# Performance work log

Measured on AMD Instinct MI355X. Metric: run time of the kernel, lower is better.

Reference implementation:

```python
import jax, jax.numpy as jnp
import numpy as np

B, T, D, K = 4, 4096, 384, 64

def setup_inputs() -> dict:
    key = jax.random.key(0)
    k1, k2, k3, k4 = jax.random.split(key, 4)
    x = jax.random.normal(k1, (B, T, D), dtype=jnp.float32)
    # nn.Linear weights stored as (out_features, in_features); y = x @ W.T
    Wk = jax.random.normal(k2, (K, D), dtype=jnp.float32) * (1.0 / np.sqrt(D))
    Wq = jax.random.normal(k3, (K, D), dtype=jnp.float32) * (1.0 / np.sqrt(D))
    Wv = jax.random.normal(k4, (D, D), dtype=jnp.float32) * (1.0 / np.sqrt(D))
    return {"x": x, "Wk": Wk, "Wq": Wq, "Wv": Wv}

def reference(x, Wk, Wq, Wv):
    # x: (B,T,D)
    k = jnp.einsum('btd,kd->btk', x, Wk)   # (B,T,K)
    q = jnp.einsum('btd,kd->btk', x, Wq)   # (B,T,K)
    v = jnp.einsum('btd,ed->bte', x, Wv)   # (B,T,D)
    scores = jnp.einsum('btk,bsk->bts', q, k)  # (B,T,T)
    Tq = x.shape[1]
    causal = jnp.tril(jnp.ones((Tq, Tq), dtype=bool))[None, :, :]
    scores = jnp.where(causal, scores, -jnp.inf)
    w = jax.nn.softmax(scores / jnp.sqrt(jnp.asarray(Wk.shape[0], scores.dtype)), axis=-1)
    return jnp.einsum('bts,bsd->btd', w, v)  # (B,T,D)
```

## Files before the change

### kernel.cpp

```cpp
#include <hip/hip_runtime.h>


#define TT 4096
#define DD 384

#define OWKA 0
#define OWQA 24576
#define OWVB 49152
#define OYK  196608
#define OYQ  1245184
#define OVT  2293760
#define OOB  8585216
#define OLF  11730944
#define OLB  11747328

#define C_EXP 0.18033688011112042f

typedef __bf16 bf16x8 __attribute__((ext_vector_type(8)));
typedef float f32x16 __attribute__((ext_vector_type(16)));
typedef unsigned short u16x4 __attribute__((ext_vector_type(4)));

__device__ __forceinline__ unsigned short f2bf(float f) {
  unsigned int u = __builtin_bit_cast(unsigned int, f);
  u += 0x7FFFu + ((u >> 16) & 1u);
  return (unsigned short)(u >> 16);
}

__device__ __forceinline__ float bf2f(unsigned short s) {
  unsigned int u = ((unsigned int)s) << 16;
  return __builtin_bit_cast(float, u);
}

__device__ __forceinline__ bf16x8 ldb8(const unsigned short* p) {
  return *reinterpret_cast<const bf16x8*>(p);
}

__global__ __launch_bounds__(256) void convert_w(
    const float* __restrict__ Wk, const float* __restrict__ Wq,
    const float* __restrict__ Wv, unsigned short* __restrict__ ws) {
  int g = blockIdx.x * 256 + threadIdx.x;
  int row = g / 96;
  int fin = (g - row * 96) * 4;
  const float* src;
  unsigned short* dstbase;
  int m;
  if (row < 64)       { src = Wk + row * 384;         dstbase = ws + OWKA; m = row; }
  else if (row < 128) { src = Wq + (row - 64) * 384;  dstbase = ws + OWQA; m = row - 64; }
  else                { src = Wv + (row - 128) * 384; dstbase = ws + OWVB; m = row - 128; }
  float4 f = *reinterpret_cast<const float4*>(src + fin);
  u16x4 o;
  o[0] = f2bf(f.x); o[1] = f2bf(f.y); o[2] = f2bf(f.z); o[3] = f2bf(f.w);
  unsigned short* dst = dstbase + (m >> 5) * 12288 + (fin >> 4) * 512
                        + ((((fin >> 3) & 1) << 5) + (m & 31)) * 8 + (fin & 7);
  *reinterpret_cast<u16x4*>(dst) = o;
}

__global__ __launch_bounds__(512) void proj_fused(
    const float* __restrict__ x, const unsigned short* __restrict__ ws_r,
    unsigned short* __restrict__ Yk, unsigned short* __restrict__ Yq,
    unsigned short* __restrict__ Vt) {
  __shared__ __align__(16) unsigned short xlds[24576];
  int tb = blockIdx.x;
  int b = tb >> 6;
  int tid = threadIdx.x;
  {
    const float* xbase = x + tb * 64 * DD;
#pragma unroll
    for (int i = 0; i < 12; i++) {
      int idx = tid + 512 * i;
      int r = idx / 96;
      int fin = (idx - r * 96) * 4;
      float4 f = *reinterpret_cast<const float4*>(xbase + idx * 4);
      u16x4 o;
      o[0] = f2bf(f.x); o[1] = f2bf(f.y); o[2] = f2bf(f.z); o[3] = f2bf(f.w);
      unsigned short* dst = xlds + (r >> 5) * 12288 + (fin >> 4) * 512
                            + ((((fin >> 3) & 1) << 5) + (r & 31)) * 8 + (fin & 7);
      *reinterpret_cast<u16x4*>(dst) = o;
    }
  }
  __syncthreads();
  int wid = tid >> 6, lane = tid & 63;
  int l31 = lane & 31, h8 = lane >> 5;
  const f32x16 fz16 = {};
  if (wid < 2) {
    const unsigned short* Wa = ws_r + (wid ? OWQA : OWKA) + lane * 8;
    unsigned short* Ysel = (wid ? Yq : Yk);
    f32x16 acc[2][2];
    acc[0][0] = fz16; acc[0][1] = fz16; acc[1][0] = fz16; acc[1][1] = fz16;
    for (int ks = 0; ks < 24; ks++) {
      bf16x8 a0 = ldb8(Wa + ks * 512);
      bf16x8 a1 = ldb8(Wa + 12288 + ks * 512);
      bf16x8 b0 = ldb8(xlds + ks * 512 + lane * 8);
      bf16x8 b1 = ldb8(xlds + 12288 + ks * 512 + lane * 8);
      acc[0][0] = __builtin_amdgcn_mfma_f32_32x32x16_bf16(a0, b0, acc[0][0], 0, 0, 0);
      acc[0][1] = __builtin_amdgcn_mfma_f32_32x32x16_bf16(a0, b1, acc[0][1], 0, 0, 0);
      acc[1][0] = __builtin_amdgcn_mfma_f32_32x32x16_bf16(a1, b0, acc[1][0], 0, 0, 0);
      acc[1][1] = __builtin_amdgcn_mfma_f32_32x32x16_bf16(a1, b1, acc[1][1], 0, 0, 0);
    }
#pragma unroll
    for (int mt = 0; mt < 2; mt++)
#pragma unroll
      for (int nt = 0; nt < 2; nt++) {
        int tile = b * 128 + (tb & 63) * 2 + nt;
#pragma unroll
        for (int rg = 0; rg < 4; rg++) {
          u16x4 o;
#pragma unroll
          for (int i = 0; i < 4; i++) o[i] = f2bf(acc[mt][nt][rg * 4 + i]);
          *reinterpret_cast<u16x4*>(Ysel + tile * 2048 + (mt * 2 + (rg >> 1)) * 512
                                    + (((rg & 1) << 5) + l31) * 8 + 4 * h8) = o;
        }
      }
  } else {
    int vw = wid - 2;
    const unsigned short* Wb = ws_r + OWVB + vw * 2 * 12288 + lane * 8;
    f32x16 acc[2][2];
    acc[0][0] = fz16; acc[0][1] = fz16; acc[1][0] = fz16; acc[1][1] = fz16;
    for (int ks = 0; ks < 24; ks++) {
      bf16x8 a0 = ldb8(xlds + ks * 512 + lane * 8);
      bf16x8 a1 = ldb8(xlds + 12288 + ks * 512 + lane * 8);
      bf16x8 w0 = ldb8(Wb + ks * 512);
      bf16x8 w1 = ldb8(Wb + 12288 + ks * 512);
      acc[0][0] = __builtin_amdgcn_mfma_f32_32x32x16_bf16(a0, w0, acc[0][0], 0, 0, 0);
      acc[0][1] = __builtin_amdgcn_mfma_f32_32x32x16_bf16(a0, w1, acc[0][1], 0, 0, 0);
      acc[1][0] = __builtin_amdgcn_mfma_f32_32x32x16_bf16(a1, w0, acc[1][0], 0, 0, 0);
      acc[1][1] = __builtin_amdgcn_mfma_f32_32x32x16_bf16(a1, w1, acc[1][1], 0, 0, 0);
    }
    int k128 = (tb & 63) >> 1;
#pragma unroll
    for (int t32 = 0; t32 < 2; t32++)
#pragma unroll
      for (int dt = 0; dt < 2; dt++) {
        int dti = vw * 2 + dt;
        unsigned short* vbase = Vt + ((b * 12 + dti) * 32 + k128) * 4096;
#pragma unroll
        for (int rg = 0; rg < 4; rg++) {
          u16x4 o;
#pragma unroll
          for (int i = 0; i < 4; i++) o[i] = f2bf(acc[t32][dt][rg * 4 + i]);
          int kseg = 4 * (tb & 1) + t32 * 2 + (rg >> 1);
          *reinterpret_cast<u16x4*>(vbase + kseg * 512
                                    + (((rg & 1) << 5) + l31) * 8 + 4 * h8) = o;
        }
      }
  }
}

__global__ __launch_bounds__(256, 2) void flash_attn(
    const unsigned short* __restrict__ Yk, const unsigned short* __restrict__ Yq,
    const unsigned short* __restrict__ Vt, float* __restrict__ out,
    unsigned short* __restrict__ obk, float* __restrict__ lf, float* __restrict__ lb) {
  __shared__ __align__(16) unsigned short pbuf[2][8192];
  __shared__ float lred[4][32];
  int blk = blockIdx.x;
  int b, st, kb0, kb1, mode, n128;
  if (blk < 512) {
    b = blk & 3;
    int u = blk >> 2;
    st = 127 - (u >> 1);
    n128 = (st >> 2) + 1;
    int front = (n128 + 1) >> 1;
    if ((u & 1) == 0) { kb0 = 0; kb1 = front; mode = 1; }
    else              { kb0 = front; kb1 = n128; mode = 2; }
  } else {
    int v = blk - 512;
    b = v & 3;
    st = 63 - (v >> 2);
    n128 = (st >> 2) + 1;
    kb0 = 0; kb1 = n128; mode = 0;
  }
  int wid = threadIdx.x >> 6, lane = threadIdx.x & 63;
  int l31 = lane & 31, h8 = lane >> 5;
  const f32x16 fz16 = {};
  const unsigned short* qbase = Yq + (b * 128 + st) * 2048 + lane * 8;
  bf16x8 qf[4];
#pragma unroll
  for (int ks = 0; ks < 4; ks++) qf[ks] = ldb8(qbase + ks * 512);
  f32x16 acc[3];
  acc[0] = fz16; acc[1] = fz16; acc[2] = fz16;
  float psum = 0.f;
  int qrow = st * 32 + l31;
  const unsigned short* kbase = Yk + (b * 128 + wid) * 2048 + lane * 8;
  const unsigned short* vbase = Vt + ((b * 12 + wid * 3) * 32) * 4096 + lane * 8;
#pragma unroll 1
  for (int kb = kb0; kb < kb1; kb++) {
    const unsigned short* kt = kbase + kb * 8192;
    bf16x8 kf[4];
#pragma unroll
    for (int ks = 0; ks < 4; ks++) kf[ks] = ldb8(kt + ks * 512);
    f32x16 sacc = fz16;
#pragma unroll
    for (int ks = 0; ks < 4; ks++)
      sacc = __builtin_amdgcn_mfma_f32_32x32x16_bf16(kf[ks], qf[ks], sacc, 0, 0, 0);
    int kg0 = kb * 128 + wid * 32 + 4 * h8;
    unsigned short* pw = pbuf[kb & 1];
#pragma unroll
    for (int rg = 0; rg < 4; rg++) {
      u16x4 o;
#pragma unroll
      for (int j = 0; j < 4; j++) {
        int key = kg0 + rg * 8 + j;
        float pv = (key > qrow) ? 0.f : exp2f(sacc[rg * 4 + j] * C_EXP);
        psum += pv;
        o[j] = f2bf(pv);
      }
      int g = wid * 2 + (rg >> 1);
      *reinterpret_cast<u16x4*>(pw + g * 512 + ((rg & 1) * 32 + l31) * 8 + 4 * h8) = o;
    }
    const unsigned short* vt = vbase + kb * 4096;
    bf16x8 vf0[8], vf1[8], vf2[8];
#pragma unroll
    for (int g = 0; g < 8; g++) vf0[g] = ldb8(vt + g * 512);
#pragma unroll
    for (int g = 0; g < 8; g++) vf1[g] = ldb8(vt + 32 * 4096 + g * 512);
#pragma unroll
    for (int g = 0; g < 8; g++) vf2[g] = ldb8(vt + 64 * 4096 + g * 512);
    __syncthreads();
    bf16x8 pf[8];
#pragma unroll
    for (int g = 0; g < 8; g++) pf[g] = ldb8(pw + g * 512 + lane * 8);
#pragma unroll
    for (int g = 0; g < 8; g++) {
      acc[0] = __builtin_amdgcn_mfma_f32_32x32x16_bf16(vf0[g], pf[g], acc[0], 0, 0, 0);
      acc[1] = __builtin_amdgcn_mfma_f32_32x32x16_bf16(vf1[g], pf[g], acc[1], 0, 0, 0);
      acc[2] = __builtin_amdgcn_mfma_f32_32x32x16_bf16(vf2[g], pf[g], acc[2], 0, 0, 0);
    }
  }
  psum += __shfl_xor(psum, 32);
  if (h8 == 0) lred[wid][l31] = psum;
  __syncthreads();
  float lt = lred[0][l31] + lred[1][l31] + lred[2][l31] + lred[3][l31];
  if (mode == 0) {
    float inv = 1.0f / lt;
    float* ob = out + (b * TT + st * 32 + l31) * DD + wid * 96;
#pragma unroll
    for (int dt = 0; dt < 3; dt++)
#pragma unroll
      for (int rg = 0; rg < 4; rg++) {
        float4 o4;
        o4.x = acc[dt][rg * 4 + 0] * inv; o4.y = acc[dt][rg * 4 + 1] * inv;
        o4.z = acc[dt][rg * 4 + 2] * inv; o4.w = acc[dt][rg * 4 + 3] * inv;
        *reinterpret_cast<float4*>(ob + dt * 32 + rg * 8 + h8 * 4) = o4;
      }
  } else if (mode == 1) {
    float* ob = out + (b * TT + st * 32 + l31) * DD + wid * 96;
#pragma unroll
    for (int dt = 0; dt < 3; dt++)
#pragma unroll
      for (int rg = 0; rg < 4; rg++) {
        float4 o4;
        o4.x = acc[dt][rg * 4 + 0]; o4.y = acc[dt][rg * 4 + 1];
        o4.z = acc[dt][rg * 4 + 2]; o4.w = acc[dt][rg * 4 + 3];
        *reinterpret_cast<float4*>(ob + dt * 32 + rg * 8 + h8 * 4) = o4;
      }
    if (wid == 0 && h8 == 0) lf[(b * 64 + st - 64) * 32 + l31] = lt;
  } else {
    unsigned short* ob = obk + ((b * 64 + st - 64) * 32 + l31) * DD + wid * 96;
#pragma unroll
    for (int dt = 0; dt < 3; dt++)
#pragma unroll
      for (int rg = 0; rg < 4; rg++) {
        u16x4 o;
#pragma unroll
        for (int i = 0; i < 4; i++) o[i] = f2bf(acc[dt][rg * 4 + i]);
        *reinterpret_cast<u16x4*>(ob + dt * 32 + rg * 8 + h8 * 4) = o;
      }
    if (wid == 0 && h8 == 0) lb[(b * 64 + st - 64) * 32 + l31] = lt;
  }
}

__global__ __launch_bounds__(256) void merge_split(
    float* __restrict__ out, const unsigned short* __restrict__ obk,
    const float* __restrict__ lf, const float* __restrict__ lb) {
  int blk = blockIdx.x;
  int b = blk >> 6, s = blk & 63;
  int tid = threadIdx.x;
  int q = tid >> 3, g = tid & 7;
  int base = (b * 64 + s) * 32 + q;
  float inv = 1.0f / (lf[base] + lb[base]);
  float* ro = out + (b * TT + (64 + s) * 32 + q) * DD + g * 48;
  const unsigned short* po = obk + base * DD + g * 48;
#pragma unroll
  for (int i = 0; i < 12; i++) {
    float4 o4 = *reinterpret_cast<const float4*>(ro + i * 4);
    u16x4 p = *reinterpret_cast<const u16x4*>(po + i * 4);
    o4.x = (o4.x + bf2f(p[0])) * inv;
    o4.y = (o4.y + bf2f(p[1])) * inv;
    o4.z = (o4.z + bf2f(p[2])) * inv;
    o4.w = (o4.w + bf2f(p[3])) * inv;
    *reinterpret_cast<float4*>(ro + i * 4) = o4;
  }
}

extern "C" void kernel_launch(void* const* d_in, const int* in_sizes, int n_in,
                              void* d_out, int out_size, void* d_ws, size_t ws_size,
                              hipStream_t stream) {
  const float* x  = (const float*)d_in[0];
  const float* Wk = (const float*)d_in[1];
  const float* Wq = (const float*)d_in[2];
  const float* Wv = (const float*)d_in[3];
  unsigned short* ws = (unsigned short*)d_ws;
  unsigned short* Yk  = ws + OYK;
  unsigned short* Yq  = ws + OYQ;
  unsigned short* Vt  = ws + OVT;
  unsigned short* obk = ws + OOB;
  float* lf = (float*)(ws + OLF);
  float* lb = (float*)(ws + OLB);

  convert_w<<<192, 256, 0, stream>>>(Wk, Wq, Wv, ws);
  proj_fused<<<256, 512, 0, stream>>>(x, ws, Yk, Yq, Vt);
  flash_attn<<<768, 256, 0, stream>>>(Yk, Yq, Vt, (float*)d_out, obk, lf, lb);
  merge_split<<<256, 256, 0, stream>>>((float*)d_out, obk, lf, lb);
}
```

Baseline: 162.0 us.

## Process two query tiles per attention block with 1/2/3-way key splits

Each flash-attention block now handles 64 query rows (two 32-row tiles) that share each loaded K/V tile. This halves K and V traffic per query and doubles MFMA work per V fragment load. Work is rebalanced with variable 1/2/3-way key-range splits, using separate bf16 partial buffers and a merge that sums up to three pieces. The causal mask is applied only on the last key block. Separately, the LDS layout for x in the projection kernel gets a rotation swizzle with 8-wide stores to reduce bank conflicts. The cost is more accumulator registers per thread and a heavier merge step.

Result: no change. 159.6 us (-1.5%).

```diff
diff --git a/kernel.cpp b/kernel.cpp
--- a/kernel.cpp
+++ b/kernel.cpp
@@ -10,15 +10,18 @@
 #define OYK  196608
 #define OYQ  1245184
 #define OVT  2293760
-#define OOB  8585216
-#define OLF  11730944
-#define OLB  11747328
+#define OB1  8585216
+#define OB2  13303808
+#define OL0  14876672
+#define OL1  14909440
+#define OL2  14942208
 
 #define C_EXP 0.18033688011112042f
 
 typedef __bf16 bf16x8 __attribute__((ext_vector_type(8)));
 typedef float f32x16 __attribute__((ext_vector_type(16)));
 typedef unsigned short u16x4 __attribute__((ext_vector_type(4)));
+typedef unsigned short u16x8 __attribute__((ext_vector_type(8)));
 
 __device__ __forceinline__ unsigned short f2bf(float f) {
   unsigned int u = __builtin_bit_cast(unsigned int, f);
@@ -66,16 +69,19 @@
   {
     const float* xbase = x + tb * 64 * DD;
 #pragma unroll
-    for (int i = 0; i < 12; i++) {
-      int idx = tid + 512 * i;
-      int r = idx / 96;
-      int fin = (idx - r * 96) * 4;
-      float4 f = *reinterpret_cast<const float4*>(xbase + idx * 4);
-      u16x4 o;
-      o[0] = f2bf(f.x); o[1] = f2bf(f.y); o[2] = f2bf(f.z); o[3] = f2bf(f.w);
-      unsigned short* dst = xlds + (r >> 5) * 12288 + (fin >> 4) * 512
-                            + ((((fin >> 3) & 1) << 5) + (r & 31)) * 8 + (fin & 7);
-      *reinterpret_cast<u16x4*>(dst) = o;
+    for (int i = 0; i < 6; i++) {
+      int j = tid + 512 * i;
+      int r = j / 48, g8 = j - r * 48;
+      const float* src = xbase + r * DD + g8 * 8;
+      float4 f0 = *reinterpret_cast<const float4*>(src);
+      float4 f1 = *reinterpret_cast<const float4*>(src + 4);
+      u16x8 o;
+      o[0] = f2bf(f0.x); o[1] = f2bf(f0.y); o[2] = f2bf(f0.z); o[3] = f2bf(f0.w);
+      o[4] = f2bf(f1.x); o[5] = f2bf(f1.y); o[6] = f2bf(f1.z); o[7] = f2bf(f1.w);
+      int ks = g8 >> 1, hb = g8 & 1;
+      int r31s = ((r & 31) + ks) & 31;
+      unsigned short* dst = xlds + (r >> 5) * 12288 + ks * 512 + (hb * 32 + r31s) * 8;
+      *reinterpret_cast<u16x8*>(dst) = o;
     }
   }
   __syncthreads();
@@ -88,10 +94,11 @@
     f32x16 acc[2][2];
     acc[0][0] = fz16; acc[0][1] = fz16; acc[1][0] = fz16; acc[1][1] = fz16;
     for (int ks = 0; ks < 24; ks++) {
+      int sl = (lane & 32) | ((lane + ks) & 31);
       bf16x8 a0 = ldb8(Wa + ks * 512);
       bf16x8 a1 = ldb8(Wa + 12288 + ks * 512);
-      bf16x8 b0 = ldb8(xlds + ks * 512 + lane * 8);
-      bf16x8 b1 = ldb8(xlds + 12288 + ks * 512 + lane * 8);
+      bf16x8 b0 = ldb8(xlds + ks * 512 + sl * 8);
+      bf16x8 b1 = ldb8(xlds + 12288 + ks * 512 + sl * 8);
       acc[0][0] = __builtin_amdgcn_mfma_f32_32x32x16_bf16(a0, b0, acc[0][0], 0, 0, 0);
       acc[0][1] = __builtin_amdgcn_mfma_f32_32x32x16_bf16(a0, b1, acc[0][1], 0, 0, 0);
       acc[1][0] = __builtin_amdgcn_mfma_f32_32x32x16_bf16(a1, b0, acc[1][0], 0, 0, 0);
@@ -117,8 +124,9 @@
     f32x16 acc[2][2];
     acc[0][0] = fz16; acc[0][1] = fz16; acc[1][0] = fz16; acc[1][1] = fz16;
     for (int ks = 0; ks < 24; ks++) {
-      bf16x8 a0 = ldb8(xlds + ks * 512 + lane * 8);
-      bf16x8 a1 = ldb8(xlds + 12288 + ks * 512 + lane * 8);
+      int sl = (lane & 32) | ((lane + ks) & 31);
+      bf16x8 a0 = ldb8(xlds + ks * 512 + sl * 8);
+      bf16x8 a1 = ldb8(xlds + 12288 + ks * 512 + sl * 8);
       bf16x8 w0 = ldb8(Wb + ks * 512);
       bf16x8 w1 = ldb8(Wb + 12288 + ks * 512);
       acc[0][0] = __builtin_amdgcn_mfma_f32_32x32x16_bf16(a0, w0, acc[0][0], 0, 0, 0);
@@ -149,63 +157,69 @@
 __global__ __launch_bounds__(256, 2) void flash_attn(
     const unsigned short* __restrict__ Yk, const unsigned short* __restrict__ Yq,
     const unsigned short* __restrict__ Vt, float* __restrict__ out,
-    unsigned short* __restrict__ obk, float* __restrict__ lf, float* __restrict__ lb) {
-  __shared__ __align__(16) unsigned short pbuf[2][8192];
-  __shared__ float lred[4][32];
+    unsigned short* __restrict__ ob1, unsigned short* __restrict__ ob2,
+    float* __restrict__ l0, float* __restrict__ l1, float* __restrict__ l2) {
+  __shared__ __align__(16) unsigned short pbuf[2][2][8192];
+  __shared__ float lred[4][2][32];
   int blk = blockIdx.x;
-  int b, st, kb0, kb1, mode, n128;
-  if (blk < 512) {
-    b = blk & 3;
-    int u = blk >> 2;
-    st = 127 - (u >> 1);
-    n128 = (st >> 2) + 1;
-    int front = (n128 + 1) >> 1;
-    if ((u & 1) == 0) { kb0 = 0; kb1 = front; mode = 1; }
-    else              { kb0 = front; kb1 = n128; mode = 2; }
-  } else {
-    int v = blk - 512;
-    b = v & 3;
-    st = 63 - (v >> 2);
-    n128 = (st >> 2) + 1;
-    kb0 = 0; kb1 = n128; mode = 0;
-  }
+  int b = blk & 3;
+  int u = blk >> 2;
+  int st, piece, P;
+  if (u < 32)       { st = 47 - (u >> 1); piece = u & 1; P = 2; }
+  else if (u < 80)  { int v = u - 32; st = 63 - v / 3; piece = v % 3; P = 3; }
+  else if (u < 88)  { st = 15 - (u - 80); piece = 0; P = 1; }
+  else if (u < 120) { int v = u - 88; st = 31 - (v >> 1); piece = v & 1; P = 2; }
+  else              { st = 7 - (u - 120); piece = 0; P = 1; }
+  int n128 = (st >> 1) + 1;
+  int kb0 = (n128 * piece) / P, kb1 = (n128 * (piece + 1)) / P;
   int wid = threadIdx.x >> 6, lane = threadIdx.x & 63;
   int l31 = lane & 31, h8 = lane >> 5;
   const f32x16 fz16 = {};
-  const unsigned short* qbase = Yq + (b * 128 + st) * 2048 + lane * 8;
-  bf16x8 qf[4];
-#pragma unroll
-  for (int ks = 0; ks < 4; ks++) qf[ks] = ldb8(qbase + ks * 512);
-  f32x16 acc[3];
-  acc[0] = fz16; acc[1] = fz16; acc[2] = fz16;
-  float psum = 0.f;
-  int qrow = st * 32 + l31;
-  const unsigned short* kbase = Yk + (b * 128 + wid) * 2048 + lane * 8;
+  bf16x8 qf[2][4];
+#pragma unroll
+  for (int qt = 0; qt < 2; qt++)
+#pragma unroll
+    for (int ks = 0; ks < 4; ks++)
+      qf[qt][ks] = ldb8(Yq + (b * 128 + st * 2 + qt) * 2048 + ks * 512 + lane * 8);
+  f32x16 acc[3][2];
+#pragma unroll
+  for (int dt = 0; dt < 3; dt++) { acc[dt][0] = fz16; acc[dt][1] = fz16; }
+  float psum0 = 0.f, psum1 = 0.f;
+  const unsigned short* kbase = Yk + (b * 128) * 2048 + lane * 8;
   const unsigned short* vbase = Vt + ((b * 12 + wid * 3) * 32) * 4096 + lane * 8;
 #pragma unroll 1
   for (int kb = kb0; kb < kb1; kb++) {
-    const unsigned short* kt = kbase + kb * 8192;
+    const unsigned short* kt = kbase + (kb * 4 + wid) * 2048;
     bf16x8 kf[4];
 #pragma unroll
     for (int ks = 0; ks < 4; ks++) kf[ks] = ldb8(kt + ks * 512);
-    f32x16 sacc = fz16;
-#pragma unroll
-    for (int ks = 0; ks < 4; ks++)
-      sacc = __builtin_amdgcn_mfma_f32_32x32x16_bf16(kf[ks], qf[ks], sacc, 0, 0, 0);
+    f32x16 s0 = fz16, s1 = fz16;
+#pragma unroll
+    for (int ks = 0; ks < 4; ks++) {
+      s0 = __builtin_amdgcn_mfma_f32_32x32x16_bf16(kf[ks], qf[0][ks], s0, 0, 0, 0);
+      s1 = __builtin_amdgcn_mfma_f32_32x32x16_bf16(kf[ks], qf[1][ks], s1, 0, 0, 0);
+    }
     int kg0 = kb * 128 + wid * 32 + 4 * h8;
-    unsigned short* pw = pbuf[kb & 1];
-#pragma unroll
-    for (int rg = 0; rg < 4; rg++) {
-      u16x4 o;
-#pragma unroll
-      for (int j = 0; j < 4; j++) {
-        int key = kg0 + rg * 8 + j;
-        float pv = (key > qrow) ? 0.f : exp2f(sacc[rg * 4 + j] * C_EXP);
-        psum += pv;
-        o[j] = f2bf(pv);
+    bool lastb = (kb == n128 - 1);
+    unsigned short* pw = &pbuf[kb & 1][0][0];
+#pragma unroll
+    for (int qt = 0; qt < 2; qt++) {
+      int qrow = st * 64 + qt * 32 + l31;
+#pragma unroll
+      for (int rg = 0; rg < 4; rg++) {
+        u16x4 o;
+#pragma unroll
+        for (int j = 0; j < 4; j++) {
+          float sv = qt ? s1[rg * 4 + j] : s0[rg * 4 + j];
+          int key = kg0 + rg * 8 + j;
+          float pv = (lastb && key > qrow) ? 0.f : exp2f(sv * C_EXP);
+          if (qt) psum1 += pv; else psum0 += pv;
+          o[j] = f2bf(pv);
+        }
+        int g = wid * 2 + (rg >> 1);
+        *reinterpret_cast<u16x4*>(pw + qt * 8192 + g * 512
+                                  + ((rg & 1) * 32 + l31) * 8 + 4 * h8) = o;
       }
-      int g = wid * 2 + (rg >> 1);
-      *reinterpret_cast<u16x4*>(pw + g * 512 + ((rg & 1) * 32 + l31) * 8 + 4 * h8) = o;
     }
     const unsigned short* vt = vbase + kb * 4096;
     bf16x8 vf0[8], vf1[8], vf2[8];
@@ -216,78 +230,109 @@
 #pragma unroll
     for (int g = 0; g < 8; g++) vf2[g] = ldb8(vt + 64 * 4096 + g * 512);
     __syncthreads();
-    bf16x8 pf[8];
-#pragma unroll
-    for (int g = 0; g < 8; g++) pf[g] = ldb8(pw + g * 512 + lane * 8);
 #pragma unroll
     for (int g = 0; g < 8; g++) {
-      acc[0] = __builtin_amdgcn_mfma_f32_32x32x16_bf16(vf0[g], pf[g], acc[0], 0, 0, 0);
-      acc[1] = __builtin_amdgcn_mfma_f32_32x32x16_bf16(vf1[g], pf[g], acc[1], 0, 0, 0);
-      acc[2] = __builtin_amdgcn_mfma_f32_32x32x16_bf16(vf2[g], pf[g], acc[2], 0, 0, 0);
-    }
-  }
-  psum += __shfl_xor(psum, 32);
-  if (h8 == 0) lred[wid][l31] = psum;
+      bf16x8 pf0 = ldb8(pw + g * 512 + lane * 8);
+      bf16x8 pf1 = ldb8(pw + 8192 + g * 512 + lane * 8);
+      acc[0][0] = __builtin_amdgcn_mfma_f32_32x32x16_bf16(vf0[g], pf0, acc[0][0], 0, 0, 0);
+      acc[0][1] = __builtin_amdgcn_mfma_f32_32x32x16_bf16(vf0[g], pf1, acc[0][1], 0, 0, 0);
+      acc[1][0] = __builtin_amdgcn_mfma_f32_32x32x16_bf16(vf1[g], pf0, acc[1][0], 0, 0, 0);
+      acc[1][1] = __builtin_amdgcn_mfma_f32_32x32x16_bf16(vf1[g], pf1, acc[1][1], 0, 0, 0);
+      acc[2][0] = __builtin_amdgcn_mfma_f32_32x32x16_bf16(vf2[g], pf0, acc[2][0], 0, 0, 0);
+      acc[2][1] = __builtin_amdgcn_mfma_f32_32x32x16_bf16(vf2[g], pf1, acc[2][1], 0, 0, 0);
+    }
+  }
+  psum0 += __shfl_xor(psum0, 32);
+  psum1 += __shfl_xor(psum1, 32);
+  if (h8 == 0) { lred[wid][0][l31] = psum0; lred[wid][1][l31] = psum1; }
   __syncthreads();
-  float lt = lred[0][l31] + lred[1][l31] + lred[2][l31] + lred[3][l31];
-  if (mode == 0) {
-    float inv = 1.0f / lt;
-    float* ob = out + (b * TT + st * 32 + l31) * DD + wid * 96;
-#pragma unroll
-    for (int dt = 0; dt < 3; dt++)
-#pragma unroll
-      for (int rg = 0; rg < 4; rg++) {
-        float4 o4;
-        o4.x = acc[dt][rg * 4 + 0] * inv; o4.y = acc[dt][rg * 4 + 1] * inv;
-        o4.z = acc[dt][rg * 4 + 2] * inv; o4.w = acc[dt][rg * 4 + 3] * inv;
-        *reinterpret_cast<float4*>(ob + dt * 32 + rg * 8 + h8 * 4) = o4;
-      }
-  } else if (mode == 1) {
-    float* ob = out + (b * TT + st * 32 + l31) * DD + wid * 96;
-#pragma unroll
-    for (int dt = 0; dt < 3; dt++)
-#pragma unroll
-      for (int rg = 0; rg < 4; rg++) {
-        float4 o4;
-        o4.x = acc[dt][rg * 4 + 0]; o4.y = acc[dt][rg * 4 + 1];
-        o4.z = acc[dt][rg * 4 + 2]; o4.w = acc[dt][rg * 4 + 3];
-        *reinterpret_cast<float4*>(ob + dt * 32 + rg * 8 + h8 * 4) = o4;
-      }
-    if (wid == 0 && h8 == 0) lf[(b * 64 + st - 64) * 32 + l31] = lt;
+  float lt0 = lred[0][0][l31] + lred[1][0][l31] + lred[2][0][l31] + lred[3][0][l31];
+  float lt1 = lred[0][1][l31] + lred[1][1][l31] + lred[2][1][l31] + lred[3][1][l31];
+  if (P == 1) {
+    float inv0 = 1.0f / lt0, inv1 = 1.0f / lt1;
+#pragma unroll
+    for (int qt = 0; qt < 2; qt++) {
+      float inv = qt ? inv1 : inv0;
+      float* ob = out + (b * TT + st * 64 + qt * 32 + l31) * DD + wid * 96;
+#pragma unroll
+      for (int dt = 0; dt < 3; dt++)
+#pragma unroll
+        for (int rg = 0; rg < 4; rg++) {
+          float4 o4;
+          o4.x = acc[dt][qt][rg * 4 + 0] * inv; o4.y = acc[dt][qt][rg * 4 + 1] * inv;
+          o4.z = acc[dt][qt][rg * 4 + 2] * inv; o4.w = acc[dt][qt][rg * 4 + 3] * inv;
+          *reinterpret_cast<float4*>(ob + dt * 32 + rg * 8 + h8 * 4) = o4;
+        }
+    }
+  } else if (piece == 0) {
+#pragma unroll
+    for (int qt = 0; qt < 2; qt++) {
+      float* ob = out + (b * TT + st * 64 + qt * 32 + l31) * DD + wid * 96;
+#pragma unroll
+      for (int dt = 0; dt < 3; dt++)
+#pragma unroll
+        for (int rg = 0; rg < 4; rg++) {
+          float4 o4;
+          o4.x = acc[dt][qt][rg * 4 + 0]; o4.y = acc[dt][qt][rg * 4 + 1];
+          o4.z = acc[dt][qt][rg * 4 + 2]; o4.w = acc[dt][qt][rg * 4 + 3];
+          *reinterpret_cast<float4*>(ob + dt * 32 + rg * 8 + h8 * 4) = o4;
+        }
+    }
+    if (wid == 0 && h8 == 0) {
+      l0[(b * 64 + st) * 64 + l31] = lt0;
+      l0[(b * 64 + st) * 64 + 32 + l31] = lt1;
+    }
   } else {
-    unsigned short* ob = obk + ((b * 64 + st - 64) * 32 + l31) * DD + wid * 96;
-#pragma unroll
-    for (int dt = 0; dt < 3; dt++)
-#pragma unroll
-      for (int rg = 0; rg < 4; rg++) {
-        u16x4 o;
-#pragma unroll
-        for (int i = 0; i < 4; i++) o[i] = f2bf(acc[dt][rg * 4 + i]);
-        *reinterpret_cast<u16x4*>(ob + dt * 32 + rg * 8 + h8 * 4) = o;
-      }
-    if (wid == 0 && h8 == 0) lb[(b * 64 + st - 64) * 32 + l31] = lt;
+    unsigned short* obp;
+    float* lp;
+    if (piece == 1) { obp = ob1 + ((b * 48 + st - 16) * 64) * DD; lp = l1; }
+    else            { obp = ob2 + ((b * 16 + st - 48) * 64) * DD; lp = l2; }
+#pragma unroll
+    for (int qt = 0; qt < 2; qt++) {
+      unsigned short* ob = obp + (qt * 32 + l31) * DD + wid * 96;
+#pragma unroll
+      for (int dt = 0; dt < 3; dt++)
+#pragma unroll
+        for (int rg = 0; rg < 4; rg++) {
+          u16x4 o;
+#pragma unroll
+          for (int i = 0; i < 4; i++) o[i] = f2bf(acc[dt][qt][rg * 4 + i]);
+          *reinterpret_cast<u16x4*>(ob + dt * 32 + rg * 8 + h8 * 4) = o;
+        }
+    }
+    if (wid == 0 && h8 == 0) {
+      lp[(b * 64 + st) * 64 + l31] = lt0;
+      lp[(b * 64 + st) * 64 + 32 + l31] = lt1;
+    }
   }
 }
 
 __global__ __launch_bounds__(256) void merge_split(
-    float* __restrict__ out, const unsigned short* __restrict__ obk,
-    const float* __restrict__ lf, const float* __restrict__ lb) {
+    float* __restrict__ out, const unsigned short* __restrict__ ob1,
+    const unsigned short* __restrict__ ob2, const float* __restrict__ l0,
+    const float* __restrict__ l1, const float* __restrict__ l2) {
   int blk = blockIdx.x;
-  int b = blk >> 6, s = blk & 63;
+  int b = blk / 48, s = blk - b * 48;
+  int st = 16 + s;
+  bool has2 = (st >= 48);
   int tid = threadIdx.x;
-  int q = tid >> 3, g = tid & 7;
-  int base = (b * 64 + s) * 32 + q;
-  float inv = 1.0f / (lf[base] + lb[base]);
-  float* ro = out + (b * TT + (64 + s) * 32 + q) * DD + g * 48;
-  const unsigned short* po = obk + base * DD + g * 48;
-#pragma unroll
-  for (int i = 0; i < 12; i++) {
+  int q = tid >> 2, seg = tid & 3;
+  int qi = (b * 64 + st) * 64 + q;
+  float lt = l0[qi] + l1[qi] + (has2 ? l2[qi] : 0.f);
+  float inv = 1.0f / lt;
+  float* ro = out + (b * TT + st * 64 + q) * DD + seg * 96;
+  const unsigned short* p1 = ob1 + ((b * 48 + s) * 64 + q) * DD + seg * 96;
+  const unsigned short* p2 = ob2 + ((b * 16 + st - 48) * 64 + q) * DD + seg * 96;
+#pragma unroll
+  for (int i = 0; i < 24; i++) {
     float4 o4 = *reinterpret_cast<const float4*>(ro + i * 4);
-    u16x4 p = *reinterpret_cast<const u16x4*>(po + i * 4);
-    o4.x = (o4.x + bf2f(p[0])) * inv;
-    o4.y = (o4.y + bf2f(p[1])) * inv;
-    o4.z = (o4.z + bf2f(p[2])) * inv;
-    o4.w = (o4.w + bf2f(p[3])) * inv;
+    u16x4 a = *reinterpret_cast<const u16x4*>(p1 + i * 4);
+    o4.x += bf2f(a[0]); o4.y += bf2f(a[1]); o4.z += bf2f(a[2]); o4.w += bf2f(a[3]);
+    if (has2) {
+      u16x4 c = *reinterpret_cast<const u16x4*>(p2 + i * 4);
+      o4.x += bf2f(c[0]); o4.y += bf2f(c[1]); o4.z += bf2f(c[2]); o4.w += bf2f(c[3]);
+    }
+    o4.x *= inv; o4.y *= inv; o4.z *= inv; o4.w *= inv;
     *reinterpret_cast<float4*>(ro + i * 4) = o4;
   }
 }
@@ -303,12 +348,14 @@
   unsigned short* Yk  = ws + OYK;
   unsigned short* Yq  = ws + OYQ;
   unsigned short* Vt  = ws + OVT;
-  unsigned short* obk = ws + OOB;
-  float* lf = (float*)(ws + OLF);
-  float* lb = (float*)(ws + OLB);
+  unsigned short* ob1 = ws + OB1;
+  unsigned short* ob2 = ws + OB2;
+  float* l0 = (float*)(ws + OL0);
+  float* l1 = (float*)(ws + OL1);
+  float* l2 = (float*)(ws + OL2);
 
   convert_w<<<192, 256, 0, stream>>>(Wk, Wq, Wv, ws);
   proj_fused<<<256, 512, 0, stream>>>(x, ws, Yk, Yq, Vt);
-  flash_attn<<<768, 256, 0, stream>>>(Yk, Yq, Vt, (float*)d_out, obk, lf, lb);
-  merge_split<<<256, 256, 0, stream>>>((float*)d_out, obk, lf, lb);
-}
+  flash_attn<<<512, 256, 0, stream>>>(Yk, Yq, Vt, (float*)d_out, ob1, ob2, l0, l1, l2);
+  merge_split<<<192, 256, 0, stream>>>((float*)d_out, ob1, ob2, l0, l1, l2);
+}
```
